# Kernel tuning notes

Measured on AMD Instinct MI355X. Metric: run time of the kernel, lower is better.

## Reference

```python
import jax, jax.numpy as jnp
import numpy as np

KERNEL = 25  # hard-coded moving-average kernel in the torch Model
HID = 128


def moving_avg(x):
    # x: [B, L, C]; edge-pad (KERNEL-1)//2 on each side along time, then mean over window
    p = (KERNEL - 1) // 2
    front = jnp.repeat(x[:, 0:1, :], p, axis=1)
    end = jnp.repeat(x[:, -1:, :], p, axis=1)
    xp = jnp.concatenate([front, x, end], axis=1)  # [B, L+2p, C]
    cs = jnp.cumsum(xp, axis=1)
    cs = jnp.concatenate([jnp.zeros_like(cs[:, :1, :]), cs], axis=1)
    return (cs[:, KERNEL:, :] - cs[:, :-KERNEL, :]) / KERNEL  # [B, L, C]


def memory_enhance(repres, memory):
    # repres: [N, 128], memory: [F, 128]
    attention = jax.nn.softmax(jnp.einsum('nd,fd->nf', repres, memory), axis=1)
    output = jnp.einsum('nf,fd->nd', attention, memory)
    return jnp.concatenate([output, repres], axis=1)  # [N, 256]


def setup_inputs() -> dict:
    key = jax.random.key(0)
    ks = jax.random.split(key, 12)
    B, L, C, P, M = 128, 720, 321, 336, 512
    s = lambda k, shape, fan: jax.random.normal(k, shape, jnp.float32) * (1.0 / np.sqrt(fan))
    return {
        'x': jax.random.normal(ks[0], (B, L, C), jnp.float32),
        'W_s1': s(ks[1], (HID, L), L), 'b_s1': jnp.zeros((HID,), jnp.float32),
        'W_s2': s(ks[2], (P, 2 * HID), 2 * HID), 'b_s2': jnp.zeros((P,), jnp.float32),
        'W_t1': s(ks[3], (HID, L), L), 'b_t1': jnp.zeros((HID,), jnp.float32),
        'W_t2': s(ks[4], (P, 2 * HID), 2 * HID), 'b_t2': jnp.zeros((P,), jnp.float32),
        'mem_S': s(ks[5], (M, HID), HID),
        'mem_T': s(ks[6], (M, HID), HID),
    }


def reference(x, W_s1, b_s1, W_s2, b_s2, W_t1, b_t1, W_t2, b_t2, mem_S, mem_T):
    B, L, C = x.shape
    trend = moving_avg(x)                 # [B, L, C]
    seasonal = x - trend
    seasonal = jnp.transpose(seasonal, (0, 2, 1))  # [B, C, L]
    trend = jnp.transpose(trend, (0, 2, 1))

    def branch(init, W1, b1, mem, W2, b2):
        r = jax.nn.sigmoid(jnp.einsum('bcl,hl->bch', init, W1) + b1)  # [B, C, 128]
        r = r.reshape(-1, HID)
        r = memory_enhance(r, mem)                                    # [N, 256]
        r = r.reshape(B, C, 2 * HID)
        return jnp.einsum('bcd,pd->bcp', r, W2) + b2                  # [B, C, P]

    seasonal_out = branch(seasonal, W_s1, b_s1, mem_S, W_s2, b_s2)
    trend_out = branch(trend, W_t1, b_t1, mem_T, W_t2, b_t2)
    return jnp.transpose(seasonal_out + trend_out, (0, 2, 1))  # [B, P, C]
```

## Files before the change

### kernel.cpp

```cpp
#include <hip/hip_runtime.h>
#include <math.h>

#define BB 128
#define LL 720
#define CC 321
#define HH 128
#define PP 336
#define MM 512
#define LPAD 768

typedef __attribute__((ext_vector_type(8))) short bf16x8;
typedef __attribute__((ext_vector_type(4))) float f32x4;

__device__ __forceinline__ short f2bf(float x) {
  unsigned u = __builtin_bit_cast(unsigned, x);
  u = (u + 0x7FFFu + ((u >> 16) & 1u)) >> 16;
  return (short)u;
}

__device__ __forceinline__ int packpos(int kw) {
  return ((kw & 15) >> 2) * 8 + (kw >> 4) * 4 + (kw & 3);
}

__device__ __forceinline__ void gload_lds16(const short* g, short* l) {
  __builtin_amdgcn_global_load_lds(
      (const __attribute__((address_space(1))) unsigned int*)g,
      (__attribute__((address_space(3))) unsigned int*)l, 16, 0, 0);
}

__global__ void weff_kernel(const float* __restrict__ Ws1,
                            const float* __restrict__ Wt1,
                            short* __restrict__ wimg) {
  int idx = blockIdx.x * 256 + threadIdx.x;
  if (idx >= HH * LPAD) return;
  int j = idx % LPAD, h = idx / LPAD;
  int s = j >> 6, kw6 = j & 63, g = kw6 >> 5, kw = kw6 & 31;
  int half = kw >> 4, lg = (kw >> 2) & 3, jj = kw & 3;
  size_t base = ((size_t)(s * 128 + h)) * 128 + half * 4 + jj;
  int slotS = g * 8 + ((0 + lg) ^ (h & 7));
  int slotT = g * 8 + ((4 + lg) ^ (h & 7));
  if (j >= LL) {
    wimg[base + slotS * 8] = 0;
    wimg[base + slotT * 8] = 0;
    return;
  }
  float ss = 0.f, st = 0.f;
  if (j == 0) {
    for (int l = 0; l <= 12; ++l) {
      float w = 13.f - (float)l;
      ss += w * Ws1[h * LL + l];
      st += w * Wt1[h * LL + l];
    }
  } else if (j == LL - 1) {
    for (int d = 0; d <= 12; ++d) {
      float w = 13.f - (float)d;
      ss += w * Ws1[h * LL + LL - 1 - d];
      st += w * Wt1[h * LL + LL - 1 - d];
    }
  } else {
    int lo = j - 12 < 0 ? 0 : j - 12;
    int hi = j + 12 > LL - 1 ? LL - 1 : j + 12;
    for (int l = lo; l <= hi; ++l) {
      ss += Ws1[h * LL + l];
      st += Wt1[h * LL + l];
    }
  }
  ss *= (1.f / 25.f);
  st *= (1.f / 25.f);
  wimg[base + slotS * 8] = f2bf(Ws1[h * LL + j] - ss);
  wimg[base + slotT * 8] = f2bf(st);
}

__global__ void memstage_kernel(const float* __restrict__ memS,
                                const float* __restrict__ memT,
                                short* __restrict__ stgS,
                                short* __restrict__ stgT) {
  int e = blockIdx.x * 256 + threadIdx.x;
  int br = e >> 14;
  int s = e & 16383;
  const float* src = br ? memT : memS;
  short* dst = br ? stgT : stgS;
  int tt = s >> 11;
  int c = s & 2047;
  int row = c >> 4, slot = c & 15;
  int sp = slot ^ (row & 7);
  int k = sp >> 2, lg = sp & 3;
  int ft = tt >> 1;
  short out[8];
  if ((tt & 1) == 0) {
    const float* r0 = src + (size_t)(ft * 128 + row) * 128 + k * 32 + lg * 4;
#pragma unroll
    for (int j = 0; j < 4; ++j) {
      out[j] = f2bf(r0[j]);
      out[j + 4] = f2bf(r0[16 + j]);
    }
  } else {
    int fbase = ft * 128 + k * 32 + lg * 4;
#pragma unroll
    for (int j = 0; j < 4; ++j) {
      out[j] = f2bf(src[(size_t)(fbase + j) * 128 + row]);
      out[j + 4] = f2bf(src[(size_t)(fbase + 16 + j) * 128 + row]);
    }
  }
  short4 a = make_short4(out[0], out[1], out[2], out[3]);
  short4 b = make_short4(out[4], out[5], out[6], out[7]);
  *(short4*)&dst[(size_t)s * 8] = a;
  *(short4*)&dst[(size_t)s * 8 + 4] = b;
}

__global__ void w2cvt_kernel(const float* __restrict__ Ws2,
                             const float* __restrict__ Wt2,
                             const float* __restrict__ bs2,
                             const float* __restrict__ bt2,
                             short* __restrict__ W2b, float* __restrict__ b2) {
  int i = blockIdx.x * 256 + threadIdx.x;
  if (i < PP) b2[i] = bs2[i] + bt2[i];
  if (i >= PP * 512) return;
  int p = i >> 9, k = i & 511;
  float v = (k < 256) ? Ws2[p * 256 + k] : Wt2[p * 256 + (k - 256)];
  W2b[p * 512 + (k >> 5) * 32 + packpos(k & 31)] = f2bf(v);
}

__global__ __launch_bounds__(256, 2) void gemm1_mfma(
    const float* __restrict__ x, const short* __restrict__ wimg,
    const float* __restrict__ bs1, const float* __restrict__ bt1,
    short* __restrict__ r2s, short* __restrict__ r2t) {
  __shared__ __align__(16) short wlds[2][16384];
  __shared__ __align__(16) short xlds[2][4096];
  int tid = threadIdx.x;
  int w = tid >> 6, l = tid & 63, lr = l & 15, lg = l >> 4;
  int ngrp = w >> 1, hhalf = w & 1, hb = hhalf * 64;
  int nb = blockIdx.x * 64;
  int cc0 = ngrp * 32 + lr, cc1 = cc0 + 16;
  int n0 = nb + cc0, n1 = nb + cc1;

  int xcc = l;
  int kg = w;
  int xn = nb + xcc;
  int xb_ = xn / CC, xc_ = xn - xb_ * CC;
  const float* xptr = x + (size_t)xb_ * (LL * CC) + xc_;
  int xr = xcc >> 1, xodd = xcc & 1, xhalf = kg >> 1;
  int lgA = (kg & 1) * 2;
  int dxA = xr * 64 + (((xodd * 4 + lgA) ^ (xr & 7))) * 8 + xhalf * 4;
  int dxB = xr * 64 + (((xodd * 4 + lgA + 1) ^ (xr & 7))) * 8 + xhalf * 4;

  const short* wsrc0 = wimg + (size_t)(w * 512 + l * 8);

  f32x4 acc[2][4][2];
#pragma unroll
  for (int br = 0; br < 2; ++br)
#pragma unroll
    for (int i = 0; i < 4; ++i)
#pragma unroll
      for (int rt = 0; rt < 2; ++rt) acc[br][i][rt] = (f32x4){0.f, 0.f, 0.f, 0.f};

  {
#pragma unroll
    for (int i = 0; i < 8; ++i)
      gload_lds16(wsrc0 + i * 2048, &wlds[0][i * 2048 + w * 512]);
    float x0[16];
#pragma unroll
    for (int g = 0; g < 2; ++g)
#pragma unroll
      for (int m = 0; m < 8; ++m)
        x0[g * 8 + m] = xptr[(size_t)(g * 32 + kg * 8 + m) * CC];
#pragma unroll
    for (int g = 0; g < 2; ++g) {
      short4 a = make_short4(f2bf(x0[g * 8 + 0]), f2bf(x0[g * 8 + 1]),
                             f2bf(x0[g * 8 + 2]), f2bf(x0[g * 8 + 3]));
      short4 b = make_short4(f2bf(x0[g * 8 + 4]), f2bf(x0[g * 8 + 5]),
                             f2bf(x0[g * 8 + 6]), f2bf(x0[g * 8 + 7]));
      *(short4*)&xlds[0][g * 2048 + dxA] = a;
      *(short4*)&xlds[0][g * 2048 + dxB] = b;
    }
  }
  __syncthreads();

  int r0 = cc0 >> 1, r1 = cc1 >> 1;
  int sl0 = (((cc0 & 1) * 4 + lg) ^ (r0 & 7)) * 8;
  int sl1 = (((cc1 & 1) * 4 + lg) ^ (r1 & 7)) * 8;

  int cur = 0;
  for (int s = 0; s < 12; ++s) {
    float xn_[16];
    if (s < 11) {
      int k0 = (s + 1) * 64;
#pragma unroll
      for (int g = 0; g < 2; ++g)
#pragma unroll
        for (int m = 0; m < 8; ++m) {
          int k = k0 + g * 32 + kg * 8 + m;
          xn_[g * 8 + m] = (k < LL) ? xptr[(size_t)k * CC] : 0.f;
        }
      const short* ws = wsrc0 + (size_t)(s + 1) * 16384;
#pragma unroll
      for (int i = 0; i < 8; ++i)
        gload_lds16(ws + i * 2048, &wlds[cur ^ 1][i * 2048 + w * 512]);
    }

    const short* tw = &wlds[cur][0];
    const short* tx = &xlds[cur][0];
#pragma unroll
    for (int g = 0; g < 2; ++g) {
      bf16x8 bx0 = *(const bf16x8*)&tx[g * 2048 + r0 * 64 + sl0];
      bf16x8 bx1 = *(const bf16x8*)&tx[g * 2048 + r1 * 64 + sl1];
#pragma unroll
      for (int ht = 0; ht < 4; ++ht) {
        int h = hb + ht * 16 + lr;
        bf16x8 aS = *(const bf16x8*)&tw[h * 128 + (g * 8 + (lg ^ (h & 7))) * 8];
        bf16x8 aT =
            *(const bf16x8*)&tw[h * 128 + (g * 8 + ((4 + lg) ^ (h & 7))) * 8];
        acc[0][ht][0] =
            __builtin_amdgcn_mfma_f32_16x16x32_bf16(aS, bx0, acc[0][ht][0], 0, 0, 0);
        acc[0][ht][1] =
            __builtin_amdgcn_mfma_f32_16x16x32_bf16(aS, bx1, acc[0][ht][1], 0, 0, 0);
        acc[1][ht][0] =
            __builtin_amdgcn_mfma_f32_16x16x32_bf16(aT, bx0, acc[1][ht][0], 0, 0, 0);
        acc[1][ht][1] =
            __builtin_amdgcn_mfma_f32_16x16x32_bf16(aT, bx1, acc[1][ht][1], 0, 0, 0);
      }
    }

    if (s < 11) {
      short* txn = &xlds[cur ^ 1][0];
#pragma unroll
      for (int g = 0; g < 2; ++g) {
        short4 a = make_short4(f2bf(xn_[g * 8 + 0]), f2bf(xn_[g * 8 + 1]),
                               f2bf(xn_[g * 8 + 2]), f2bf(xn_[g * 8 + 3]));
        short4 b = make_short4(f2bf(xn_[g * 8 + 4]), f2bf(xn_[g * 8 + 5]),
                               f2bf(xn_[g * 8 + 6]), f2bf(xn_[g * 8 + 7]));
        *(short4*)&txn[g * 2048 + dxA] = a;
        *(short4*)&txn[g * 2048 + dxB] = b;
      }
    }
    __syncthreads();
    cur ^= 1;
  }

#pragma unroll
  for (int rt = 0; rt < 2; ++rt) {
    int n = rt ? n1 : n0;
    short* rowS = r2s + (size_t)n * 256 + 128;
    short* rowT = r2t + (size_t)n * 256 + 128;
#pragma unroll
    for (int ht = 0; ht < 4; ++ht) {
      int h = hb + ht * 16 + lg * 4;
      int hbase = hb + ht * 16;
      int dst = (hbase >> 5) * 32 + lg * 8 + ((hbase >> 4) & 1) * 4;
      float4 bS = *(const float4*)&bs1[h];
      float4 bT = *(const float4*)&bt1[h];
      const float* pbS = &bS.x;
      const float* pbT = &bT.x;
      short4 ss, st;
      short* ps = &ss.x;
      short* pt = &st.x;
#pragma unroll
      for (int j = 0; j < 4; ++j) {
        ps[j] = f2bf(1.f / (1.f + __expf(-(acc[0][ht][rt][j] + pbS[j]))));
        pt[j] = f2bf(1.f / (1.f + __expf(-(acc[1][ht][rt][j] + pbT[j]))));
      }
      *(short4*)&rowS[dst] = ss;
      *(short4*)&rowT[dst] = st;
    }
  }
}

__global__ __launch_bounds__(256) void memenh_mfma(
    const short* __restrict__ stgS, const short* __restrict__ stgT,
    short* __restrict__ r2s, short* __restrict__ r2t) {
  int br = blockIdx.y;
  const short* stg = br ? stgT : stgS;
  short* r2 = br ? r2t : r2s;

  __shared__ __align__(16) short buf[2][16384];
  int tid = threadIdx.x;
  int l = tid & 63, lr = l & 15, lg = l >> 4;
  int wbase = tid & 192;
  int n = blockIdx.x * 64 + (tid >> 6) * 16 + lr;

  bf16x8 brag[4];
  {
    const short* rb = r2 + (size_t)n * 256 + 128;
#pragma unroll
    for (int k = 0; k < 4; ++k)
      brag[k] = *(const bf16x8*)&rb[k * 32 + lg * 8];
  }

#define STAGE(t, bsel)                                                        \
  {                                                                           \
    const short* g = stg + (size_t)(t)*16384;                                 \
    _Pragma("unroll") for (int i = 0; i < 8; ++i) {                           \
      gload_lds16(g + (size_t)(i * 256 + tid) * 8,                            \
                  &buf[bsel][(i * 256 + wbase) * 8]);                         \
    }                                                                         \
  }

  STAGE(0, 0);
  __syncthreads();

  f32x4 accO[8];
#pragma unroll
  for (int i = 0; i < 8; ++i) accO[i] = (f32x4){0.f, 0.f, 0.f, 0.f};
  bf16x8 pb[4];
  float ssum = 0.f;
  int cur = 0;

#pragma unroll
  for (int t = 0; t < 8; ++t) {
    if (t < 7) STAGE(t + 1, cur ^ 1);
    const short* tb = &buf[cur][0];
    if ((t & 1) == 0) {
      f32x4 sc[8];
#pragma unroll
      for (int ft16 = 0; ft16 < 8; ++ft16) {
        f32x4 a = {0.f, 0.f, 0.f, 0.f};
#pragma unroll
        for (int k = 0; k < 4; ++k) {
          int row = ft16 * 16 + lr;
          int slot = (4 * k + lg) ^ (row & 7);
          bf16x8 af = *(const bf16x8*)&tb[row * 128 + slot * 8];
          a = __builtin_amdgcn_mfma_f32_16x16x32_bf16(af, brag[k], a, 0, 0, 0);
        }
        sc[ft16] = a;
      }
#pragma unroll
      for (int i = 0; i < 8; ++i) {
        f32x4 v = sc[i];
#pragma unroll
        for (int j = 0; j < 4; ++j) {
          float e = __expf(v[j]);
          v[j] = e;
          ssum += e;
        }
        sc[i] = v;
      }
#pragma unroll
      for (int t4 = 0; t4 < 4; ++t4) {
        f32x4 e0 = sc[2 * t4], e1 = sc[2 * t4 + 1];
        bf16x8 f;
        f[0] = f2bf(e0[0]); f[1] = f2bf(e0[1]);
        f[2] = f2bf(e0[2]); f[3] = f2bf(e0[3]);
        f[4] = f2bf(e1[0]); f[5] = f2bf(e1[1]);
        f[6] = f2bf(e1[2]); f[7] = f2bf(e1[3]);
        pb[t4] = f;
      }
    } else {
#pragma unroll
      for (int dt = 0; dt < 8; ++dt) {
#pragma unroll
        for (int k = 0; k < 4; ++k) {
          int row = dt * 16 + lr;
          int slot = (4 * k + lg) ^ (row & 7);
          bf16x8 af = *(const bf16x8*)&tb[row * 128 + slot * 8];
          accO[dt] =
              __builtin_amdgcn_mfma_f32_16x16x32_bf16(af, pb[k], accO[dt], 0, 0, 0);
        }
      }
    }
    __syncthreads();
    cur ^= 1;
  }
#undef STAGE

  ssum += __shfl_xor(ssum, 16);
  ssum += __shfl_xor(ssum, 32);
  float inv = 1.f / ssum;
  short* rowO = r2 + (size_t)n * 256;
#pragma unroll
  for (int dt = 0; dt < 8; ++dt) {
    short4 o;
    o.x = f2bf(accO[dt][0] * inv);
    o.y = f2bf(accO[dt][1] * inv);
    o.z = f2bf(accO[dt][2] * inv);
    o.w = f2bf(accO[dt][3] * inv);
    *(short4*)&rowO[(dt >> 1) * 32 + lg * 8 + (dt & 1) * 4] = o;
  }
}

__global__ __launch_bounds__(512) void gemm2_mfma(
    const short* __restrict__ r2s, const short* __restrict__ r2t,
    const short* __restrict__ W2b,
    const float* __restrict__ b2,
    float* __restrict__ out) {
  __shared__ __align__(16) short w2lds[2][112 * 40];
  int tid = threadIdx.x;
  int w = tid >> 6, l = tid & 63, lr = l & 15, lg = l >> 4;
  int p0 = blockIdx.y * 112;
  int n = blockIdx.x * 128 + w * 16 + lr;
  int b = n / CC, c = n - b * CC;
  const short* rs = r2s + (size_t)n * 256;
  const short* rt = r2t + (size_t)n * 256;

  bool dostage = tid < 448;
  int row = tid >> 2, q = tid & 3;
  const short* gW = W2b + (size_t)(p0 + row) * 512 + q * 8;
  int doff = row * 40 + q * 8;

  f32x4 acc[7];
#pragma unroll
  for (int i = 0; i < 7; ++i) acc[i] = (f32x4){0.f, 0.f, 0.f, 0.f};

  if (dostage) *(int4*)&w2lds[0][doff] = *(const int4*)gW;
  __syncthreads();

  int cur = 0;
  for (int step = 0; step < 16; ++step) {
    int k0 = step * 32;
    const short* rrow = ((k0 < 256) ? rs : rt) + (k0 & 255);
    bf16x8 bfr = *(const bf16x8*)&rrow[lg * 8];
    int4 nxt = {0, 0, 0, 0};
    if (step < 15 && dostage) nxt = *(const int4*)(gW + (step + 1) * 32);
    const short* tw = &w2lds[cur][0];
#pragma unroll
    for (int pt = 0; pt < 7; ++pt) {
      bf16x8 a = *(const bf16x8*)&tw[(pt * 16 + lr) * 40 + lg * 8];
      acc[pt] = __builtin_amdgcn_mfma_f32_16x16x32_bf16(a, bfr, acc[pt], 0, 0, 0);
    }
    if (step < 15 && dostage) *(int4*)&w2lds[cur ^ 1][doff] = nxt;
    __syncthreads();
    cur ^= 1;
  }

  size_t obase = (size_t)b * ((size_t)PP * CC) + c;
#pragma unroll
  for (int pt = 0; pt < 7; ++pt) {
    int p = p0 + pt * 16 + lg * 4;
    float4 bias = *(const float4*)&b2[p];
    const float* pb = &bias.x;
#pragma unroll
    for (int j = 0; j < 4; ++j) {
      out[obase + (size_t)(p + j) * CC] = acc[pt][j] + pb[j];
    }
  }
}

extern "C" void kernel_launch(void* const* d_in, const int* in_sizes, int n_in,
                              void* d_out, int out_size, void* d_ws, size_t ws_size,
                              hipStream_t stream) {
  const float* x    = (const float*)d_in[0];
  const float* Ws1  = (const float*)d_in[1];
  const float* bs1  = (const float*)d_in[2];
  const float* Ws2  = (const float*)d_in[3];
  const float* bs2  = (const float*)d_in[4];
  const float* Wt1  = (const float*)d_in[5];
  const float* bt1  = (const float*)d_in[6];
  const float* Wt2  = (const float*)d_in[7];
  const float* bt2  = (const float*)d_in[8];
  const float* memS = (const float*)d_in[9];
  const float* memT = (const float*)d_in[10];
  float* out = (float*)d_out;

  const size_t N = (size_t)BB * CC;
  short* r2s  = (short*)d_ws;
  short* r2t  = r2s + N * 256;
  short* wimg = r2t + N * 256;
  short* stgS = wimg + (size_t)12 * 128 * 128;
  short* stgT = stgS + (size_t)16384 * 8;
  short* W2b  = stgT + (size_t)16384 * 8;
  float* b2   = (float*)(W2b + (size_t)PP * 512);

  weff_kernel<<<(HH * LPAD) / 256, 256, 0, stream>>>(Ws1, Wt1, wimg);
  memstage_kernel<<<128, 256, 0, stream>>>(memS, memT, stgS, stgT);
  w2cvt_kernel<<<(PP * 512) / 256, 256, 0, stream>>>(Ws2, Wt2, bs2, bt2, W2b, b2);

  gemm1_mfma<<<642, 256, 0, stream>>>(x, wimg, bs1, bt1, r2s, r2t);

  dim3 g3(642, 2);
  memenh_mfma<<<g3, 256, 0, stream>>>(stgS, stgT, r2s, r2t);

  dim3 g2(321, 3);
  gemm2_mfma<<<g2, 512, 0, stream>>>(r2s, r2t, W2b, b2, out);
}
```

Baseline: 141.7 us.

## Shrink gemm1 tile to 32 columns and K-step 32 for more occupancy

Restructures the first GEMM so each block handles 32 columns instead of 64 and steps through K in chunks of 32 (23 steps) rather than 64. Each warp now computes a single branch (seasonal or trend) rather than both, which halves LDS buffers and accumulators and raises the launch bound to 4 blocks per CU with twice as many blocks. The weight image layout is repacked to match the 32-wide K chunks. The aim is better latency hiding and CU load balance, at the cost of lower per-block reuse of the weight tile, more synchronisation steps, and the weights being re-read from L2 by twice as many blocks.

```diff
diff --git a/kernel.cpp b/kernel.cpp
--- a/kernel.cpp
+++ b/kernel.cpp
@@ -7,7 +7,7 @@
 #define HH 128
 #define PP 336
 #define MM 512
-#define LPAD 768
+#define NSTEP 23
 
 typedef __attribute__((ext_vector_type(8))) short bf16x8;
 typedef __attribute__((ext_vector_type(4))) float f32x4;
@@ -32,13 +32,13 @@
                             const float* __restrict__ Wt1,
                             short* __restrict__ wimg) {
   int idx = blockIdx.x * 256 + threadIdx.x;
-  if (idx >= HH * LPAD) return;
-  int j = idx % LPAD, h = idx / LPAD;
-  int s = j >> 6, kw6 = j & 63, g = kw6 >> 5, kw = kw6 & 31;
+  if (idx >= HH * NSTEP * 32) return;
+  int j = idx % (NSTEP * 32), h = idx / (NSTEP * 32);
+  int s = j >> 5, kw = j & 31;
   int half = kw >> 4, lg = (kw >> 2) & 3, jj = kw & 3;
-  size_t base = ((size_t)(s * 128 + h)) * 128 + half * 4 + jj;
-  int slotS = g * 8 + ((0 + lg) ^ (h & 7));
-  int slotT = g * 8 + ((4 + lg) ^ (h & 7));
+  size_t base = ((size_t)(s * 128 + h)) * 64 + half * 4 + jj;
+  int slotS = (0 + lg) ^ (h & 7);
+  int slotT = (4 + lg) ^ (h & 7);
   if (j >= LL) {
     wimg[base + slotS * 8] = 0;
     wimg[base + slotT * 8] = 0;
@@ -121,146 +121,107 @@
   W2b[p * 512 + (k >> 5) * 32 + packpos(k & 31)] = f2bf(v);
 }
 
-__global__ __launch_bounds__(256, 2) void gemm1_mfma(
+__global__ __launch_bounds__(256, 4) void gemm1_mfma(
     const float* __restrict__ x, const short* __restrict__ wimg,
     const float* __restrict__ bs1, const float* __restrict__ bt1,
     short* __restrict__ r2s, short* __restrict__ r2t) {
-  __shared__ __align__(16) short wlds[2][16384];
-  __shared__ __align__(16) short xlds[2][4096];
+  __shared__ __align__(16) short wbuf[2][8192];
+  __shared__ __align__(16) short xbuf[2][1024];
   int tid = threadIdx.x;
   int w = tid >> 6, l = tid & 63, lr = l & 15, lg = l >> 4;
-  int ngrp = w >> 1, hhalf = w & 1, hb = hhalf * 64;
-  int nb = blockIdx.x * 64;
-  int cc0 = ngrp * 32 + lr, cc1 = cc0 + 16;
-  int n0 = nb + cc0, n1 = nb + cc1;
-
-  int xcc = l;
-  int kg = w;
-  int xn = nb + xcc;
+  int br = w >> 1, hb = (w & 1) * 64;
+  int nb = blockIdx.x * 32;
+
+  int xcol = tid & 31, krow = tid >> 5;
+  int xn = nb + xcol;
   int xb_ = xn / CC, xc_ = xn - xb_ * CC;
   const float* xptr = x + (size_t)xb_ * (LL * CC) + xc_;
-  int xr = xcc >> 1, xodd = xcc & 1, xhalf = kg >> 1;
-  int lgA = (kg & 1) * 2;
-  int dxA = xr * 64 + (((xodd * 4 + lgA) ^ (xr & 7))) * 8 + xhalf * 4;
-  int dxB = xr * 64 + (((xodd * 4 + lgA + 1) ^ (xr & 7))) * 8 + xhalf * 4;
-
-  const short* wsrc0 = wimg + (size_t)(w * 512 + l * 8);
-
-  f32x4 acc[2][4][2];
-#pragma unroll
-  for (int br = 0; br < 2; ++br)
+  int xrow = xcol >> 1;
+  int xslot = ((xcol & 1) * 4 + (krow & 3)) ^ (xrow & 7);
+  int xdst = xrow * 64 + xslot * 8 + (krow >> 2) * 4;
+
+  const short* wsrc = wimg + (size_t)w * 2048 + l * 8;
+
+  f32x4 acc[4][2];
+#pragma unroll
+  for (int i = 0; i < 4; ++i)
+#pragma unroll
+    for (int g = 0; g < 2; ++g) acc[i][g] = (f32x4){0.f, 0.f, 0.f, 0.f};
+
+  {
 #pragma unroll
     for (int i = 0; i < 4; ++i)
-#pragma unroll
-      for (int rt = 0; rt < 2; ++rt) acc[br][i][rt] = (f32x4){0.f, 0.f, 0.f, 0.f};
-
-  {
-#pragma unroll
-    for (int i = 0; i < 8; ++i)
-      gload_lds16(wsrc0 + i * 2048, &wlds[0][i * 2048 + w * 512]);
-    float x0[16];
-#pragma unroll
-    for (int g = 0; g < 2; ++g)
-#pragma unroll
-      for (int m = 0; m < 8; ++m)
-        x0[g * 8 + m] = xptr[(size_t)(g * 32 + kg * 8 + m) * CC];
+      gload_lds16(wsrc + i * 512, &wbuf[0][w * 2048 + i * 512]);
+    float xf[4];
+#pragma unroll
+    for (int j = 0; j < 4; ++j) xf[j] = xptr[(size_t)(krow * 4 + j) * CC];
+    short4 v = make_short4(f2bf(xf[0]), f2bf(xf[1]), f2bf(xf[2]), f2bf(xf[3]));
+    *(short4*)&xbuf[0][xdst] = v;
+  }
+  __syncthreads();
+
+  int cur = 0;
+  for (int s = 0; s < NSTEP; ++s) {
+    float xf[4];
+    if (s < NSTEP - 1) {
+      int kbase = (s + 1) * 32 + krow * 4;
+#pragma unroll
+      for (int j = 0; j < 4; ++j) {
+        int k = kbase + j;
+        xf[j] = (k < LL) ? xptr[(size_t)k * CC] : 0.f;
+      }
+      const short* ws = wsrc + (size_t)(s + 1) * 8192;
+#pragma unroll
+      for (int i = 0; i < 4; ++i)
+        gload_lds16(ws + i * 512, &wbuf[cur ^ 1][w * 2048 + i * 512]);
+    }
+
+    const short* tw = &wbuf[cur][0];
+    const short* tx = &xbuf[cur][0];
+    bf16x8 bx[2];
 #pragma unroll
     for (int g = 0; g < 2; ++g) {
-      short4 a = make_short4(f2bf(x0[g * 8 + 0]), f2bf(x0[g * 8 + 1]),
-                             f2bf(x0[g * 8 + 2]), f2bf(x0[g * 8 + 3]));
-      short4 b = make_short4(f2bf(x0[g * 8 + 4]), f2bf(x0[g * 8 + 5]),
-                             f2bf(x0[g * 8 + 6]), f2bf(x0[g * 8 + 7]));
-      *(short4*)&xlds[0][g * 2048 + dxA] = a;
-      *(short4*)&xlds[0][g * 2048 + dxB] = b;
-    }
-  }
-  __syncthreads();
-
-  int r0 = cc0 >> 1, r1 = cc1 >> 1;
-  int sl0 = (((cc0 & 1) * 4 + lg) ^ (r0 & 7)) * 8;
-  int sl1 = (((cc1 & 1) * 4 + lg) ^ (r1 & 7)) * 8;
-
-  int cur = 0;
-  for (int s = 0; s < 12; ++s) {
-    float xn_[16];
-    if (s < 11) {
-      int k0 = (s + 1) * 64;
-#pragma unroll
-      for (int g = 0; g < 2; ++g)
-#pragma unroll
-        for (int m = 0; m < 8; ++m) {
-          int k = k0 + g * 32 + kg * 8 + m;
-          xn_[g * 8 + m] = (k < LL) ? xptr[(size_t)k * CC] : 0.f;
-        }
-      const short* ws = wsrc0 + (size_t)(s + 1) * 16384;
-#pragma unroll
-      for (int i = 0; i < 8; ++i)
-        gload_lds16(ws + i * 2048, &wlds[cur ^ 1][i * 2048 + w * 512]);
-    }
-
-    const short* tw = &wlds[cur][0];
-    const short* tx = &xlds[cur][0];
-#pragma unroll
-    for (int g = 0; g < 2; ++g) {
-      bf16x8 bx0 = *(const bf16x8*)&tx[g * 2048 + r0 * 64 + sl0];
-      bf16x8 bx1 = *(const bf16x8*)&tx[g * 2048 + r1 * 64 + sl1];
-#pragma unroll
-      for (int ht = 0; ht < 4; ++ht) {
-        int h = hb + ht * 16 + lr;
-        bf16x8 aS = *(const bf16x8*)&tw[h * 128 + (g * 8 + (lg ^ (h & 7))) * 8];
-        bf16x8 aT =
-            *(const bf16x8*)&tw[h * 128 + (g * 8 + ((4 + lg) ^ (h & 7))) * 8];
-        acc[0][ht][0] =
-            __builtin_amdgcn_mfma_f32_16x16x32_bf16(aS, bx0, acc[0][ht][0], 0, 0, 0);
-        acc[0][ht][1] =
-            __builtin_amdgcn_mfma_f32_16x16x32_bf16(aS, bx1, acc[0][ht][1], 0, 0, 0);
-        acc[1][ht][0] =
-            __builtin_amdgcn_mfma_f32_16x16x32_bf16(aT, bx0, acc[1][ht][0], 0, 0, 0);
-        acc[1][ht][1] =
-            __builtin_amdgcn_mfma_f32_16x16x32_bf16(aT, bx1, acc[1][ht][1], 0, 0, 0);
-      }
-    }
-
-    if (s < 11) {
-      short* txn = &xlds[cur ^ 1][0];
-#pragma unroll
-      for (int g = 0; g < 2; ++g) {
-        short4 a = make_short4(f2bf(xn_[g * 8 + 0]), f2bf(xn_[g * 8 + 1]),
-                               f2bf(xn_[g * 8 + 2]), f2bf(xn_[g * 8 + 3]));
-        short4 b = make_short4(f2bf(xn_[g * 8 + 4]), f2bf(xn_[g * 8 + 5]),
-                               f2bf(xn_[g * 8 + 6]), f2bf(xn_[g * 8 + 7]));
-        *(short4*)&txn[g * 2048 + dxA] = a;
-        *(short4*)&txn[g * 2048 + dxB] = b;
-      }
+      int cc = g * 16 + lr;
+      int row = cc >> 1;
+      int slot = ((cc & 1) * 4 + lg) ^ (row & 7);
+      bx[g] = *(const bf16x8*)&tx[row * 64 + slot * 8];
+    }
+#pragma unroll
+    for (int ht = 0; ht < 4; ++ht) {
+      int h = hb + ht * 16 + lr;
+      int slot = (br * 4 + lg) ^ (h & 7);
+      bf16x8 a = *(const bf16x8*)&tw[h * 64 + slot * 8];
+      acc[ht][0] =
+          __builtin_amdgcn_mfma_f32_16x16x32_bf16(a, bx[0], acc[ht][0], 0, 0, 0);
+      acc[ht][1] =
+          __builtin_amdgcn_mfma_f32_16x16x32_bf16(a, bx[1], acc[ht][1], 0, 0, 0);
+    }
+
+    if (s < NSTEP - 1) {
+      short4 v = make_short4(f2bf(xf[0]), f2bf(xf[1]), f2bf(xf[2]), f2bf(xf[3]));
+      *(short4*)&xbuf[cur ^ 1][xdst] = v;
     }
     __syncthreads();
     cur ^= 1;
   }
 
-#pragma unroll
-  for (int rt = 0; rt < 2; ++rt) {
-    int n = rt ? n1 : n0;
-    short* rowS = r2s + (size_t)n * 256 + 128;
-    short* rowT = r2t + (size_t)n * 256 + 128;
-#pragma unroll
-    for (int ht = 0; ht < 4; ++ht) {
-      int h = hb + ht * 16 + lg * 4;
-      int hbase = hb + ht * 16;
-      int dst = (hbase >> 5) * 32 + lg * 8 + ((hbase >> 4) & 1) * 4;
-      float4 bS = *(const float4*)&bs1[h];
-      float4 bT = *(const float4*)&bt1[h];
-      const float* pbS = &bS.x;
-      const float* pbT = &bT.x;
-      short4 ss, st;
-      short* ps = &ss.x;
-      short* pt = &st.x;
-#pragma unroll
-      for (int j = 0; j < 4; ++j) {
-        ps[j] = f2bf(1.f / (1.f + __expf(-(acc[0][ht][rt][j] + pbS[j]))));
-        pt[j] = f2bf(1.f / (1.f + __expf(-(acc[1][ht][rt][j] + pbT[j]))));
-      }
-      *(short4*)&rowS[dst] = ss;
-      *(short4*)&rowT[dst] = st;
+  const float* bias = br ? bt1 : bs1;
+  short* r2 = br ? r2t : r2s;
+#pragma unroll
+  for (int ht = 0; ht < 4; ++ht) {
+    int h0 = hb + ht * 16 + lg * 4;
+    int dst = (h0 >> 5) * 32 + lg * 8 + ((h0 >> 4) & 1) * 4;
+    float4 bi = *(const float4*)&bias[h0];
+    const float* pb = &bi.x;
+#pragma unroll
+    for (int g = 0; g < 2; ++g) {
+      int n = nb + g * 16 + lr;
+      short4 v;
+      short* pv = &v.x;
+#pragma unroll
+      for (int j = 0; j < 4; ++j)
+        pv[j] = f2bf(1.f / (1.f + __expf(-(acc[ht][g][j] + pb[j]))));
+      *(short4*)&r2[(size_t)n * 256 + 128 + dst] = v;
     }
   }
 }
@@ -454,16 +415,16 @@
   short* r2s  = (short*)d_ws;
   short* r2t  = r2s + N * 256;
   short* wimg = r2t + N * 256;
-  short* stgS = wimg + (size_t)12 * 128 * 128;
+  short* stgS = wimg + (size_t)NSTEP * 128 * 64;
   short* stgT = stgS + (size_t)16384 * 8;
   short* W2b  = stgT + (size_t)16384 * 8;
   float* b2   = (float*)(W2b + (size_t)PP * 512);
 
-  weff_kernel<<<(HH * LPAD) / 256, 256, 0, stream>>>(Ws1, Wt1, wimg);
+  weff_kernel<<<(HH * NSTEP * 32 + 255) / 256, 256, 0, stream>>>(Ws1, Wt1, wimg);
   memstage_kernel<<<128, 256, 0, stream>>>(memS, memT, stgS, stgT);
   w2cvt_kernel<<<(PP * 512) / 256, 256, 0, stream>>>(Ws2, Wt2, bs2, bt2, W2b, b2);
 
-  gemm1_mfma<<<642, 256, 0, stream>>>(x, wimg, bs1, bt1, r2s, r2t);
+  gemm1_mfma<<<1284, 256, 0, stream>>>(x, wimg, bs1, bt1, r2s, r2t);
 
   dim3 g3(642, 2);
   memenh_mfma<<<g3, 256, 0, stream>>>(stgS, stgT, r2s, r2t);
```

Measured after the change: 141.6 us. About the same (-0.1%).
